# Kernel optimization log

Hardware: AMD Instinct MI355X
Metric: run time of the kernel (lower is better)

The kernel has to match this reference:

```python
import jax, jax.numpy as jnp
import numpy as np

N = 100000
E = 3200000
F_IN, H1, H2, C = 128, 64, 32, 10


def setup_inputs() -> dict:
    key = jax.random.key(0)
    ks = jax.random.split(key, 8)
    x = jax.random.normal(ks[0], (N, F_IN), dtype=jnp.float32)
    edge_index = jax.random.randint(ks[1], (2, E), 0, N, dtype=jnp.int64)
    W1 = jax.random.normal(ks[2], (F_IN, H1), dtype=jnp.float32) / np.sqrt(F_IN)
    b1 = jnp.zeros((H1,), dtype=jnp.float32)
    W2 = jax.random.normal(ks[3], (H1, H2), dtype=jnp.float32) / np.sqrt(H1)
    b2 = jnp.zeros((H2,), dtype=jnp.float32)
    Wc = jax.random.normal(ks[4], (H2, C), dtype=jnp.float32) / np.sqrt(H2)
    bc = jnp.zeros((C,), dtype=jnp.float32)
    return {"x": x, "edge_index": edge_index, "W1": W1, "b1": b1,
            "W2": W2, "b2": b2, "Wc": Wc, "bc": bc}


def gcn_conv(x, src, dst, W, b, n):
    # PyG GCNConv: x' = D^{-1/2} (A + I) D^{-1/2} (X W) + b
    h = x @ W                                        # [N, H]
    ones = jnp.ones((src.shape[0],), dtype=h.dtype)
    deg = jax.ops.segment_sum(ones, dst, num_segments=n) + 1.0  # +1 self loop
    dinv = jax.lax.rsqrt(deg)                        # deg >= 1, safe
    norm = dinv[src] * dinv[dst]                     # [E]
    msg = h[src] * norm[:, None]                     # [E, H] gather + scale
    agg = jax.ops.segment_sum(msg, dst, num_segments=n)
    # self-loop contribution: norm_ii = 1/deg_i
    out = agg + h * (dinv * dinv)[:, None]
    return out + b


def reference(x, edge_index, W1, b1, W2, b2, Wc, bc):
    n = x.shape[0]
    src, dst = edge_index[0], edge_index[1]
    h = gcn_conv(x, src, dst, W1, b1, n)
    h = jax.nn.relu(h)
    # dropout is identity in eval mode (training=False)
    h = gcn_conv(h, src, dst, W2, b2, n)
    h = jax.nn.relu(h)
    logits = h @ Wc + bc
    return jax.nn.log_softmax(logits, axis=1)
```

## Files before the change

### kernel.cpp

```cpp
#include <hip/hip_runtime.h>


#define BSHIFT 8
#define BMASK 255
#define NBUCK_MAX 512
#define TILE 4096
#define EPT 16

__device__ __forceinline__ unsigned pack_bf16(float lo, float hi) {
    unsigned ul = __float_as_uint(lo);
    ul = (ul + 0x7FFFu + ((ul >> 16) & 1u)) >> 16;
    unsigned uh = __float_as_uint(hi);
    uh = ((uh + 0x7FFFu + ((uh >> 16) & 1u)) >> 16) << 16;
    return ul | uh;
}

__global__ void k_hist(const int* __restrict__ dst, int* __restrict__ bcnt, int E) {
    __shared__ int h[NBUCK_MAX];
    for (int i = threadIdx.x; i < NBUCK_MAX; i += blockDim.x) h[i] = 0;
    __syncthreads();
    for (int e = blockIdx.x * blockDim.x + threadIdx.x; e < E; e += gridDim.x * blockDim.x)
        atomicAdd(&h[dst[e] >> BSHIFT], 1);
    __syncthreads();
    for (int i = threadIdx.x; i < NBUCK_MAX; i += blockDim.x)
        if (h[i]) atomicAdd(&bcnt[i], h[i]);
}

__global__ void k_scanb(const int* __restrict__ bcnt, int* __restrict__ bbase,
                        int* __restrict__ gcur, int E) {
    __shared__ int s[NBUCK_MAX];
    int t = threadIdx.x;
    int v = bcnt[t];
    s[t] = v;
    __syncthreads();
    for (int o = 1; o < NBUCK_MAX; o <<= 1) {
        int u = (t >= o) ? s[t - o] : 0;
        __syncthreads();
        s[t] += u;
        __syncthreads();
    }
    int ex = s[t] - v;
    bbase[t] = ex;
    gcur[t] = ex;
    if (t == NBUCK_MAX - 1) bbase[NBUCK_MAX] = E;
}

__global__ __launch_bounds__(256) void k_binA(const int* __restrict__ src,
                                              const int* __restrict__ dst,
                                              int* __restrict__ gcur,
                                              int* __restrict__ binned, int E) {
    __shared__ int hist[NBUCK_MAX];
    __shared__ int lbase[NBUCK_MAX];
    __shared__ int gdelta[NBUCK_MAX];
    __shared__ int cnt2[NBUCK_MAX];
    __shared__ int scanb[256];
    __shared__ int stage[TILE];
    __shared__ unsigned short sbucket[TILE];

    int t = threadIdx.x;
    for (int i = t; i < NBUCK_MAX; i += 256) { hist[i] = 0; cnt2[i] = 0; }
    __syncthreads();

    int tileStart = blockIdx.x * TILE;
    int cntTile = min(TILE, E - tileStart);

    int vals[EPT];
    int bks[EPT];
#pragma unroll
    for (int i = 0; i < EPT; i++) {
        int e = tileStart + t + i * 256;
        if (e < E) {
            int s = src[e], d = dst[e];
            vals[i] = s | ((d & BMASK) << 17);
            bks[i] = d >> BSHIFT;
            atomicAdd(&hist[bks[i]], 1);
        } else bks[i] = -1;
    }
    __syncthreads();

    int a0 = hist[2 * t], a1 = hist[2 * t + 1];
    int ts = a0 + a1;
    scanb[t] = ts;
    __syncthreads();
    for (int o = 1; o < 256; o <<= 1) {
        int u = (t >= o) ? scanb[t - o] : 0;
        __syncthreads();
        scanb[t] += u;
        __syncthreads();
    }
    int ex = scanb[t] - ts;
    lbase[2 * t] = ex;
    lbase[2 * t + 1] = ex + a0;
    __syncthreads();

    for (int b = t; b < NBUCK_MAX; b += 256) {
        int c = hist[b];
        int g = c ? atomicAdd(&gcur[b], c) : 0;
        gdelta[b] = g - lbase[b];
    }
#pragma unroll
    for (int i = 0; i < EPT; i++) {
        if (bks[i] >= 0) {
            int r = atomicAdd(&cnt2[bks[i]], 1);
            int slot = lbase[bks[i]] + r;
            stage[slot] = vals[i];
            sbucket[slot] = (unsigned short)bks[i];
        }
    }
    __syncthreads();
    for (int i = t; i < cntTile; i += 256) {
        int b = sbucket[i];
        binned[gdelta[b] + i] = stage[i];
    }
}

__global__ void k_rowptr(const int* __restrict__ bbase, const int* __restrict__ binned,
                         int* __restrict__ rowptr, float* __restrict__ dinv, int n, int E) {
    __shared__ int cnt[256];
    __shared__ int sc[256];
    int b = blockIdx.x, t = threadIdx.x;
    cnt[t] = 0;
    __syncthreads();
    int beg = bbase[b], end = bbase[b + 1];
    for (int i = beg + t; i < end; i += 256)
        atomicAdd(&cnt[(binned[i] >> 17) & BMASK], 1);
    __syncthreads();
    int v = cnt[t];
    sc[t] = v;
    __syncthreads();
    for (int o = 1; o < 256; o <<= 1) {
        int u = (t >= o) ? sc[t - o] : 0;
        __syncthreads();
        sc[t] += u;
        __syncthreads();
    }
    int g = (b << BSHIFT) + t;
    if (g < n) {
        rowptr[g] = beg + sc[t] - v;
        dinv[g] = rsqrtf((float)v + 1.0f);
        if (g == n - 1) rowptr[n] = E;
    }
}

__global__ void k_bucketsort(const int* __restrict__ bbase, const int* __restrict__ rowptr,
                             const int* __restrict__ binned, int* __restrict__ csr, int n) {
    __shared__ int rpl[256];
    __shared__ int lcur[256];
    int b = blockIdx.x, t = threadIdx.x;
    int lo = b << BSHIFT;
    int g = lo + t;
    rpl[t] = (g < n) ? rowptr[g] : 0;
    lcur[t] = 0;
    __syncthreads();
    int beg = bbase[b], end = bbase[b + 1];
    for (int i = beg + t; i < end; i += 256) {
        int v = binned[i];
        int ln = (v >> 17) & BMASK;
        int k = atomicAdd(&lcur[ln], 1);
        csr[rpl[ln] + k] = v & 0x1FFFF;
    }
}

template<int K, int M>
__global__ void k_gemm(const float* __restrict__ X, const float* __restrict__ W,
                       const float* __restrict__ dinv, unsigned* __restrict__ hsb, int n) {
    __shared__ float Ws[K * M];
    for (int i = threadIdx.x; i < K * M; i += blockDim.x) Ws[i] = W[i];
    __syncthreads();
    int r = blockIdx.x * blockDim.x + threadIdx.x;
    if (r >= n) return;
    float acc[M];
#pragma unroll
    for (int j = 0; j < M; j++) acc[j] = 0.f;
    const float* xr = X + (size_t)r * K;
    for (int k = 0; k < K; k += 4) {
        float4 xv = *(const float4*)(xr + k);
#pragma unroll
        for (int j = 0; j < M; j++) {
            acc[j] += xv.x * Ws[(k + 0) * M + j];
            acc[j] += xv.y * Ws[(k + 1) * M + j];
            acc[j] += xv.z * Ws[(k + 2) * M + j];
            acc[j] += xv.w * Ws[(k + 3) * M + j];
        }
    }
    float di = dinv[r];
    unsigned* hr = hsb + (size_t)r * (M / 2);
#pragma unroll
    for (int j = 0; j < M / 2; j++)
        hr[j] = pack_bf16(acc[2 * j] * di, acc[2 * j + 1] * di);
}

__global__ void k_agg64n(const int* __restrict__ rowptr, const int* __restrict__ csr,
                         const unsigned* __restrict__ hsb, const float* __restrict__ dinv,
                         const float* __restrict__ bv, float* __restrict__ out, int n) {
    int d = (blockIdx.x * blockDim.x + threadIdx.x) >> 6;
    if (d >= n) return;
    int lane = threadIdx.x & 63;
    int half = lane >> 5, l5 = lane & 31;
    int beg = rowptr[d], end = rowptr[d + 1];
    float di = dinv[d];
    float acc0 = 0.f, acc1 = 0.f;
    int base = beg;
    for (; base + 4 <= end; base += 4) {
        int sA = csr[base + half];
        int sB = csr[base + 2 + half];
        unsigned wA = hsb[(size_t)sA * 32 + l5];
        unsigned wB = hsb[(size_t)sB * 32 + l5];
        acc0 += __uint_as_float(wA << 16);
        acc1 += __uint_as_float(wA & 0xFFFF0000u);
        acc0 += __uint_as_float(wB << 16);
        acc1 += __uint_as_float(wB & 0xFFFF0000u);
    }
    for (int j = base + half; j < end; j += 2) {
        unsigned w = hsb[(size_t)csr[j] * 32 + l5];
        acc0 += __uint_as_float(w << 16);
        acc1 += __uint_as_float(w & 0xFFFF0000u);
    }
    acc0 += __shfl_xor(acc0, 32, 64);
    acc1 += __shfl_xor(acc1, 32, 64);
    if (half == 0) {
        unsigned ws = hsb[(size_t)d * 32 + l5];
        acc0 += __uint_as_float(ws << 16);
        acc1 += __uint_as_float(ws & 0xFFFF0000u);
        float v0 = fmaxf(acc0 * di + bv[2 * l5], 0.f);
        float v1 = fmaxf(acc1 * di + bv[2 * l5 + 1], 0.f);
        *(float2*)(out + (size_t)d * 64 + 2 * l5) = make_float2(v0, v1);
    }
}

__global__ void k_agg32n(const int* __restrict__ rowptr, const int* __restrict__ csr,
                         const unsigned* __restrict__ hsb, const float* __restrict__ dinv,
                         const float* __restrict__ bv, float* __restrict__ out, int n) {
    int d = (blockIdx.x * blockDim.x + threadIdx.x) >> 6;
    if (d >= n) return;
    int lane = threadIdx.x & 63;
    int quarter = lane >> 4, l4 = lane & 15;
    int beg = rowptr[d], end = rowptr[d + 1];
    float di = dinv[d];
    float acc0 = 0.f, acc1 = 0.f;
    int base = beg;
    for (; base + 8 <= end; base += 8) {
        int sA = csr[base + quarter];
        int sB = csr[base + 4 + quarter];
        unsigned wA = hsb[(size_t)sA * 16 + l4];
        unsigned wB = hsb[(size_t)sB * 16 + l4];
        acc0 += __uint_as_float(wA << 16);
        acc1 += __uint_as_float(wA & 0xFFFF0000u);
        acc0 += __uint_as_float(wB << 16);
        acc1 += __uint_as_float(wB & 0xFFFF0000u);
    }
    for (int j = base + quarter; j < end; j += 4) {
        unsigned w = hsb[(size_t)csr[j] * 16 + l4];
        acc0 += __uint_as_float(w << 16);
        acc1 += __uint_as_float(w & 0xFFFF0000u);
    }
    acc0 += __shfl_xor(acc0, 16, 64);
    acc1 += __shfl_xor(acc1, 16, 64);
    acc0 += __shfl_xor(acc0, 32, 64);
    acc1 += __shfl_xor(acc1, 32, 64);
    if (quarter == 0) {
        unsigned ws = hsb[(size_t)d * 16 + l4];
        acc0 += __uint_as_float(ws << 16);
        acc1 += __uint_as_float(ws & 0xFFFF0000u);
        float v0 = fmaxf(acc0 * di + bv[2 * l4], 0.f);
        float v1 = fmaxf(acc1 * di + bv[2 * l4 + 1], 0.f);
        *(float2*)(out + (size_t)d * 32 + 2 * l4) = make_float2(v0, v1);
    }
}

__global__ void k_classifier(const float* __restrict__ ACT, const float* __restrict__ Wc,
                             const float* __restrict__ bc, float* __restrict__ out, int n) {
    __shared__ float Wcs[32 * 10];
    __shared__ float bcs[10];
    for (int i = threadIdx.x; i < 320; i += blockDim.x) Wcs[i] = Wc[i];
    if (threadIdx.x < 10) bcs[threadIdx.x] = bc[threadIdx.x];
    __syncthreads();
    int r = blockIdx.x * blockDim.x + threadIdx.x;
    if (r >= n) return;
    const float* a = ACT + (size_t)r * 32;
    float logits[10];
#pragma unroll
    for (int c = 0; c < 10; c++) logits[c] = bcs[c];
#pragma unroll
    for (int k = 0; k < 32; k += 4) {
        float4 av = *(const float4*)(a + k);
#pragma unroll
        for (int c = 0; c < 10; c++) {
            logits[c] += av.x * Wcs[(k + 0) * 10 + c] + av.y * Wcs[(k + 1) * 10 + c]
                       + av.z * Wcs[(k + 2) * 10 + c] + av.w * Wcs[(k + 3) * 10 + c];
        }
    }
    float m = logits[0];
#pragma unroll
    for (int c = 1; c < 10; c++) m = fmaxf(m, logits[c]);
    float ssum = 0.f;
#pragma unroll
    for (int c = 0; c < 10; c++) ssum += __expf(logits[c] - m);
    float lse = m + __logf(ssum);
    float* o = out + (size_t)r * 10;
#pragma unroll
    for (int c = 0; c < 10; c++) o[c] = logits[c] - lse;
}

extern "C" void kernel_launch(void* const* d_in, const int* in_sizes, int n_in,
                              void* d_out, int out_size, void* d_ws, size_t ws_size,
                              hipStream_t stream) {
    const float* x  = (const float*)d_in[0];
    const int*   ei = (const int*)d_in[1];
    const float* W1 = (const float*)d_in[2];
    const float* b1 = (const float*)d_in[3];
    const float* W2 = (const float*)d_in[4];
    const float* b2 = (const float*)d_in[5];
    const float* Wc = (const float*)d_in[6];
    const float* bc = (const float*)d_in[7];
    float* out = (float*)d_out;

    const int N = in_sizes[0] / 128;
    const int E = in_sizes[1] / 2;
    const int* src = ei;
    const int* dst = ei + E;

    const int NBUCK = (N + BMASK) >> BSHIFT;
    const int NTILE = (E + TILE - 1) / TILE;

    char* ws = (char*)d_ws;
    size_t off = 0;
    auto alloc = [&](size_t elems) {
        void* p = ws + off;
        off += ((elems * 4 + 1023) & ~(size_t)1023);
        return p;
    };
    float*    dinv   = (float*)alloc(N);
    int*      bcnt   = (int*)alloc(NBUCK_MAX);
    int*      bbase  = (int*)alloc(NBUCK_MAX + 1);
    int*      gcur   = (int*)alloc(NBUCK_MAX);
    int*      rowptr = (int*)alloc(N + 1);
    int*      binned = (int*)alloc(E);
    int*      csr    = (int*)alloc(E);
    unsigned* hsb    = (unsigned*)alloc((size_t)N * 32);
    float*    act    = (float*)alloc((size_t)N * 64);

    hipMemsetAsync(bcnt, 0, sizeof(int) * NBUCK_MAX, stream);

    k_hist<<<512, 256, 0, stream>>>(dst, bcnt, E);
    k_scanb<<<1, NBUCK_MAX, 0, stream>>>(bcnt, bbase, gcur, E);
    k_binA<<<NTILE, 256, 0, stream>>>(src, dst, gcur, binned, E);
    k_rowptr<<<NBUCK, 256, 0, stream>>>(bbase, binned, rowptr, dinv, N, E);
    k_bucketsort<<<NBUCK, 256, 0, stream>>>(bbase, rowptr, binned, csr, N);

    k_gemm<128, 64><<<(N + 255) / 256, 256, 0, stream>>>(x, W1, dinv, hsb, N);
    k_agg64n<<<(N * 64 + 255) / 256, 256, 0, stream>>>(rowptr, csr, hsb, dinv, b1, act, N);

    k_gemm<64, 32><<<(N + 255) / 256, 256, 0, stream>>>(act, W2, dinv, hsb, N);
    k_agg32n<<<(N * 64 + 255) / 256, 256, 0, stream>>>(rowptr, csr, hsb, dinv, b2, act, N);

    k_classifier<<<(N + 255) / 256, 256, 0, stream>>>(act, Wc, bc, out, N);
}
```

Before: 429.6 us.

## Fuse rowptr and bucket sort, register-tile GEMM, vectorize aggregation gathers

```diff
diff --git a/kernel.cpp b/kernel.cpp
--- a/kernel.cpp
+++ b/kernel.cpp
@@ -101,8 +101,8 @@
 #pragma unroll
     for (int i = 0; i < EPT; i++) {
         if (bks[i] >= 0) {
-            int r = atomicAdd(&cnt2[bks[i]], 1);
-            int slot = lbase[bks[i]] + r;
+            int rr = atomicAdd(&cnt2[bks[i]], 1);
+            int slot = lbase[bks[i]] + rr;
             stage[slot] = vals[i];
             sbucket[slot] = (unsigned short)bks[i];
         }
@@ -114,12 +114,15 @@
     }
 }
 
-__global__ void k_rowptr(const int* __restrict__ bbase, const int* __restrict__ binned,
-                         int* __restrict__ rowptr, float* __restrict__ dinv, int n, int E) {
+__global__ void k_sortcsr(const int* __restrict__ bbase, const int* __restrict__ binned,
+                          int* __restrict__ rowptr, float* __restrict__ dinv,
+                          int* __restrict__ csr, int n, int E) {
     __shared__ int cnt[256];
     __shared__ int sc[256];
+    __shared__ int rpl[256];
+    __shared__ int lcur[256];
     int b = blockIdx.x, t = threadIdx.x;
-    cnt[t] = 0;
+    cnt[t] = 0; lcur[t] = 0;
     __syncthreads();
     int beg = bbase[b], end = bbase[b + 1];
     for (int i = beg + t; i < end; i += 256)
@@ -134,137 +137,213 @@
         sc[t] += u;
         __syncthreads();
     }
+    int rp = beg + sc[t] - v;
+    rpl[t] = rp;
     int g = (b << BSHIFT) + t;
     if (g < n) {
-        rowptr[g] = beg + sc[t] - v;
+        rowptr[g] = rp;
         dinv[g] = rsqrtf((float)v + 1.0f);
         if (g == n - 1) rowptr[n] = E;
     }
-}
-
-__global__ void k_bucketsort(const int* __restrict__ bbase, const int* __restrict__ rowptr,
-                             const int* __restrict__ binned, int* __restrict__ csr, int n) {
-    __shared__ int rpl[256];
-    __shared__ int lcur[256];
-    int b = blockIdx.x, t = threadIdx.x;
-    int lo = b << BSHIFT;
-    int g = lo + t;
-    rpl[t] = (g < n) ? rowptr[g] : 0;
-    lcur[t] = 0;
-    __syncthreads();
-    int beg = bbase[b], end = bbase[b + 1];
+    __syncthreads();
     for (int i = beg + t; i < end; i += 256) {
-        int v = binned[i];
-        int ln = (v >> 17) & BMASK;
+        int vv = binned[i];
+        int ln = (vv >> 17) & BMASK;
         int k = atomicAdd(&lcur[ln], 1);
-        csr[rpl[ln] + k] = v & 0x1FFFF;
+        csr[rpl[ln] + k] = vv & 0x1FFFF;
     }
 }
 
 template<int K, int M>
-__global__ void k_gemm(const float* __restrict__ X, const float* __restrict__ W,
-                       const float* __restrict__ dinv, unsigned* __restrict__ hsb, int n) {
+__global__ __launch_bounds__(256) void k_gemm(const float* __restrict__ X,
+                                              const float* __restrict__ W,
+                                              const float* __restrict__ dinv,
+                                              unsigned* __restrict__ hsb, int n) {
+    constexpr int MW = M / 4;
     __shared__ float Ws[K * M];
-    for (int i = threadIdx.x; i < K * M; i += blockDim.x) Ws[i] = W[i];
-    __syncthreads();
-    int r = blockIdx.x * blockDim.x + threadIdx.x;
-    if (r >= n) return;
-    float acc[M];
-#pragma unroll
-    for (int j = 0; j < M; j++) acc[j] = 0.f;
-    const float* xr = X + (size_t)r * K;
+    for (int i = threadIdx.x; i < K * M; i += 256) Ws[i] = W[i];
+    __syncthreads();
+    int w = threadIdx.x >> 6, lane = threadIdx.x & 63;
+    int wo = w * MW;
+    int r0 = blockIdx.x * 256 + lane;
+    float acc[4][MW];
+#pragma unroll
+    for (int i = 0; i < 4; i++)
+#pragma unroll
+        for (int j = 0; j < MW; j++) acc[i][j] = 0.f;
+
     for (int k = 0; k < K; k += 4) {
-        float4 xv = *(const float4*)(xr + k);
-#pragma unroll
-        for (int j = 0; j < M; j++) {
-            acc[j] += xv.x * Ws[(k + 0) * M + j];
-            acc[j] += xv.y * Ws[(k + 1) * M + j];
-            acc[j] += xv.z * Ws[(k + 2) * M + j];
-            acc[j] += xv.w * Ws[(k + 3) * M + j];
+        float4 xv[4];
+#pragma unroll
+        for (int i = 0; i < 4; i++) {
+            int rr = r0 + 64 * i;
+            xv[i] = (rr < n) ? *(const float4*)(X + (size_t)rr * K + k)
+                             : make_float4(0.f, 0.f, 0.f, 0.f);
         }
-    }
-    float di = dinv[r];
-    unsigned* hr = hsb + (size_t)r * (M / 2);
-#pragma unroll
-    for (int j = 0; j < M / 2; j++)
-        hr[j] = pack_bf16(acc[2 * j] * di, acc[2 * j + 1] * di);
+#pragma unroll
+        for (int kk = 0; kk < 4; kk++) {
+#pragma unroll
+            for (int j = 0; j < MW; j += 4) {
+                float4 wv = *(const float4*)&Ws[(k + kk) * M + wo + j];
+#pragma unroll
+                for (int i = 0; i < 4; i++) {
+                    float xs = (kk == 0) ? xv[i].x : (kk == 1) ? xv[i].y
+                             : (kk == 2) ? xv[i].z : xv[i].w;
+                    acc[i][j + 0] += xs * wv.x;
+                    acc[i][j + 1] += xs * wv.y;
+                    acc[i][j + 2] += xs * wv.z;
+                    acc[i][j + 3] += xs * wv.w;
+                }
+            }
+        }
+    }
+#pragma unroll
+    for (int i = 0; i < 4; i++) {
+        int rr = r0 + 64 * i;
+        if (rr < n) {
+            float di = dinv[rr];
+            unsigned p[MW / 2];
+#pragma unroll
+            for (int jj = 0; jj < MW / 2; jj++)
+                p[jj] = pack_bf16(acc[i][2 * jj] * di, acc[i][2 * jj + 1] * di);
+            unsigned* hr = hsb + (size_t)rr * (M / 2) + wo / 2;
+#pragma unroll
+            for (int jj = 0; jj < MW / 2; jj += 4)
+                *(uint4*)(hr + jj) = make_uint4(p[jj], p[jj + 1], p[jj + 2], p[jj + 3]);
+        }
+    }
 }
 
 __global__ void k_agg64n(const int* __restrict__ rowptr, const int* __restrict__ csr,
-                         const unsigned* __restrict__ hsb, const float* __restrict__ dinv,
+                         const uint4* __restrict__ hsb, const float* __restrict__ dinv,
                          const float* __restrict__ bv, float* __restrict__ out, int n) {
+    __shared__ float bs[64];
+    if (threadIdx.x < 64) bs[threadIdx.x] = bv[threadIdx.x];
+    __syncthreads();
     int d = (blockIdx.x * blockDim.x + threadIdx.x) >> 6;
     if (d >= n) return;
     int lane = threadIdx.x & 63;
-    int half = lane >> 5, l5 = lane & 31;
+    int q = lane >> 3;
+    int r = lane & 7;
     int beg = rowptr[d], end = rowptr[d + 1];
-    float di = dinv[d];
-    float acc0 = 0.f, acc1 = 0.f;
+    float acc[8];
+#pragma unroll
+    for (int i = 0; i < 8; i++) acc[i] = 0.f;
     int base = beg;
-    for (; base + 4 <= end; base += 4) {
-        int sA = csr[base + half];
-        int sB = csr[base + 2 + half];
-        unsigned wA = hsb[(size_t)sA * 32 + l5];
-        unsigned wB = hsb[(size_t)sB * 32 + l5];
-        acc0 += __uint_as_float(wA << 16);
-        acc1 += __uint_as_float(wA & 0xFFFF0000u);
-        acc0 += __uint_as_float(wB << 16);
-        acc1 += __uint_as_float(wB & 0xFFFF0000u);
-    }
-    for (int j = base + half; j < end; j += 2) {
-        unsigned w = hsb[(size_t)csr[j] * 32 + l5];
-        acc0 += __uint_as_float(w << 16);
-        acc1 += __uint_as_float(w & 0xFFFF0000u);
-    }
-    acc0 += __shfl_xor(acc0, 32, 64);
-    acc1 += __shfl_xor(acc1, 32, 64);
-    if (half == 0) {
-        unsigned ws = hsb[(size_t)d * 32 + l5];
-        acc0 += __uint_as_float(ws << 16);
-        acc1 += __uint_as_float(ws & 0xFFFF0000u);
-        float v0 = fmaxf(acc0 * di + bv[2 * l5], 0.f);
-        float v1 = fmaxf(acc1 * di + bv[2 * l5 + 1], 0.f);
-        *(float2*)(out + (size_t)d * 64 + 2 * l5) = make_float2(v0, v1);
+    for (; base + 16 <= end; base += 16) {
+        int sA = csr[base + q];
+        int sB = csr[base + 8 + q];
+        uint4 wA = hsb[(size_t)sA * 8 + r];
+        uint4 wB = hsb[(size_t)sB * 8 + r];
+        acc[0] += __uint_as_float(wA.x << 16);  acc[1] += __uint_as_float(wA.x & 0xFFFF0000u);
+        acc[2] += __uint_as_float(wA.y << 16);  acc[3] += __uint_as_float(wA.y & 0xFFFF0000u);
+        acc[4] += __uint_as_float(wA.z << 16);  acc[5] += __uint_as_float(wA.z & 0xFFFF0000u);
+        acc[6] += __uint_as_float(wA.w << 16);  acc[7] += __uint_as_float(wA.w & 0xFFFF0000u);
+        acc[0] += __uint_as_float(wB.x << 16);  acc[1] += __uint_as_float(wB.x & 0xFFFF0000u);
+        acc[2] += __uint_as_float(wB.y << 16);  acc[3] += __uint_as_float(wB.y & 0xFFFF0000u);
+        acc[4] += __uint_as_float(wB.z << 16);  acc[5] += __uint_as_float(wB.z & 0xFFFF0000u);
+        acc[6] += __uint_as_float(wB.w << 16);  acc[7] += __uint_as_float(wB.w & 0xFFFF0000u);
+    }
+    if (base + q < end) {
+        uint4 w = hsb[(size_t)csr[base + q] * 8 + r];
+        acc[0] += __uint_as_float(w.x << 16);  acc[1] += __uint_as_float(w.x & 0xFFFF0000u);
+        acc[2] += __uint_as_float(w.y << 16);  acc[3] += __uint_as_float(w.y & 0xFFFF0000u);
+        acc[4] += __uint_as_float(w.z << 16);  acc[5] += __uint_as_float(w.z & 0xFFFF0000u);
+        acc[6] += __uint_as_float(w.w << 16);  acc[7] += __uint_as_float(w.w & 0xFFFF0000u);
+    }
+    if (base + 8 + q < end) {
+        uint4 w = hsb[(size_t)csr[base + 8 + q] * 8 + r];
+        acc[0] += __uint_as_float(w.x << 16);  acc[1] += __uint_as_float(w.x & 0xFFFF0000u);
+        acc[2] += __uint_as_float(w.y << 16);  acc[3] += __uint_as_float(w.y & 0xFFFF0000u);
+        acc[4] += __uint_as_float(w.z << 16);  acc[5] += __uint_as_float(w.z & 0xFFFF0000u);
+        acc[6] += __uint_as_float(w.w << 16);  acc[7] += __uint_as_float(w.w & 0xFFFF0000u);
+    }
+#pragma unroll
+    for (int i = 0; i < 8; i++) {
+        acc[i] += __shfl_xor(acc[i], 8, 64);
+        acc[i] += __shfl_xor(acc[i], 16, 64);
+        acc[i] += __shfl_xor(acc[i], 32, 64);
+    }
+    uint4 ws = hsb[(size_t)d * 8 + r];
+    acc[0] += __uint_as_float(ws.x << 16);  acc[1] += __uint_as_float(ws.x & 0xFFFF0000u);
+    acc[2] += __uint_as_float(ws.y << 16);  acc[3] += __uint_as_float(ws.y & 0xFFFF0000u);
+    acc[4] += __uint_as_float(ws.z << 16);  acc[5] += __uint_as_float(ws.z & 0xFFFF0000u);
+    acc[6] += __uint_as_float(ws.w << 16);  acc[7] += __uint_as_float(ws.w & 0xFFFF0000u);
+    if (q == 0) {
+        float di = dinv[d];
+        float v[8];
+#pragma unroll
+        for (int i = 0; i < 8; i++) v[i] = fmaxf(acc[i] * di + bs[8 * r + i], 0.f);
+        float* o = out + (size_t)d * 64 + 8 * r;
+        *(float4*)(o + 0) = make_float4(v[0], v[1], v[2], v[3]);
+        *(float4*)(o + 4) = make_float4(v[4], v[5], v[6], v[7]);
     }
 }
 
 __global__ void k_agg32n(const int* __restrict__ rowptr, const int* __restrict__ csr,
-                         const unsigned* __restrict__ hsb, const float* __restrict__ dinv,
+                         const uint4* __restrict__ hsb, const float* __restrict__ dinv,
                          const float* __restrict__ bv, float* __restrict__ out, int n) {
+    __shared__ float bs[32];
+    if (threadIdx.x < 32) bs[threadIdx.x] = bv[threadIdx.x];
+    __syncthreads();
     int d = (blockIdx.x * blockDim.x + threadIdx.x) >> 6;
     if (d >= n) return;
     int lane = threadIdx.x & 63;
-    int quarter = lane >> 4, l4 = lane & 15;
+    int q = lane >> 2;
+    int r = lane & 3;
     int beg = rowptr[d], end = rowptr[d + 1];
-    float di = dinv[d];
-    float acc0 = 0.f, acc1 = 0.f;
+    float acc[8];
+#pragma unroll
+    for (int i = 0; i < 8; i++) acc[i] = 0.f;
     int base = beg;
-    for (; base + 8 <= end; base += 8) {
-        int sA = csr[base + quarter];
-        int sB = csr[base + 4 + quarter];
-        unsigned wA = hsb[(size_t)sA * 16 + l4];
-        unsigned wB = hsb[(size_t)sB * 16 + l4];
-        acc0 += __uint_as_float(wA << 16);
-        acc1 += __uint_as_float(wA & 0xFFFF0000u);
-        acc0 += __uint_as_float(wB << 16);
-        acc1 += __uint_as_float(wB & 0xFFFF0000u);
-    }
-    for (int j = base + quarter; j < end; j += 4) {
-        unsigned w = hsb[(size_t)csr[j] * 16 + l4];
-        acc0 += __uint_as_float(w << 16);
-        acc1 += __uint_as_float(w & 0xFFFF0000u);
-    }
-    acc0 += __shfl_xor(acc0, 16, 64);
-    acc1 += __shfl_xor(acc1, 16, 64);
-    acc0 += __shfl_xor(acc0, 32, 64);
-    acc1 += __shfl_xor(acc1, 32, 64);
-    if (quarter == 0) {
-        unsigned ws = hsb[(size_t)d * 16 + l4];
-        acc0 += __uint_as_float(ws << 16);
-        acc1 += __uint_as_float(ws & 0xFFFF0000u);
-        float v0 = fmaxf(acc0 * di + bv[2 * l4], 0.f);
-        float v1 = fmaxf(acc1 * di + bv[2 * l4 + 1], 0.f);
-        *(float2*)(out + (size_t)d * 32 + 2 * l4) = make_float2(v0, v1);
+    for (; base + 32 <= end; base += 32) {
+        int sA = csr[base + q];
+        int sB = csr[base + 16 + q];
+        uint4 wA = hsb[(size_t)sA * 4 + r];
+        uint4 wB = hsb[(size_t)sB * 4 + r];
+        acc[0] += __uint_as_float(wA.x << 16);  acc[1] += __uint_as_float(wA.x & 0xFFFF0000u);
+        acc[2] += __uint_as_float(wA.y << 16);  acc[3] += __uint_as_float(wA.y & 0xFFFF0000u);
+        acc[4] += __uint_as_float(wA.z << 16);  acc[5] += __uint_as_float(wA.z & 0xFFFF0000u);
+        acc[6] += __uint_as_float(wA.w << 16);  acc[7] += __uint_as_float(wA.w & 0xFFFF0000u);
+        acc[0] += __uint_as_float(wB.x << 16);  acc[1] += __uint_as_float(wB.x & 0xFFFF0000u);
+        acc[2] += __uint_as_float(wB.y << 16);  acc[3] += __uint_as_float(wB.y & 0xFFFF0000u);
+        acc[4] += __uint_as_float(wB.z << 16);  acc[5] += __uint_as_float(wB.z & 0xFFFF0000u);
+        acc[6] += __uint_as_float(wB.w << 16);  acc[7] += __uint_as_float(wB.w & 0xFFFF0000u);
+    }
+    if (base + q < end) {
+        uint4 w = hsb[(size_t)csr[base + q] * 4 + r];
+        acc[0] += __uint_as_float(w.x << 16);  acc[1] += __uint_as_float(w.x & 0xFFFF0000u);
+        acc[2] += __uint_as_float(w.y << 16);  acc[3] += __uint_as_float(w.y & 0xFFFF0000u);
+        acc[4] += __uint_as_float(w.z << 16);  acc[5] += __uint_as_float(w.z & 0xFFFF0000u);
+        acc[6] += __uint_as_float(w.w << 16);  acc[7] += __uint_as_float(w.w & 0xFFFF0000u);
+    }
+    if (base + 16 + q < end) {
+        uint4 w = hsb[(size_t)csr[base + 16 + q] * 4 + r];
+        acc[0] += __uint_as_float(w.x << 16);  acc[1] += __uint_as_float(w.x & 0xFFFF0000u);
+        acc[2] += __uint_as_float(w.y << 16);  acc[3] += __uint_as_float(w.y & 0xFFFF0000u);
+        acc[4] += __uint_as_float(w.z << 16);  acc[5] += __uint_as_float(w.z & 0xFFFF0000u);
+        acc[6] += __uint_as_float(w.w << 16);  acc[7] += __uint_as_float(w.w & 0xFFFF0000u);
+    }
+#pragma unroll
+    for (int i = 0; i < 8; i++) {
+        acc[i] += __shfl_xor(acc[i], 4, 64);
+        acc[i] += __shfl_xor(acc[i], 8, 64);
+        acc[i] += __shfl_xor(acc[i], 16, 64);
+        acc[i] += __shfl_xor(acc[i], 32, 64);
+    }
+    uint4 ws = hsb[(size_t)d * 4 + r];
+    acc[0] += __uint_as_float(ws.x << 16);  acc[1] += __uint_as_float(ws.x & 0xFFFF0000u);
+    acc[2] += __uint_as_float(ws.y << 16);  acc[3] += __uint_as_float(ws.y & 0xFFFF0000u);
+    acc[4] += __uint_as_float(ws.z << 16);  acc[5] += __uint_as_float(ws.z & 0xFFFF0000u);
+    acc[6] += __uint_as_float(ws.w << 16);  acc[7] += __uint_as_float(ws.w & 0xFFFF0000u);
+    if (q == 0) {
+        float di = dinv[d];
+        float v[8];
+#pragma unroll
+        for (int i = 0; i < 8; i++) v[i] = fmaxf(acc[i] * di + bs[8 * r + i], 0.f);
+        float* o = out + (size_t)d * 32 + 8 * r;
+        *(float4*)(o + 0) = make_float4(v[0], v[1], v[2], v[3]);
+        *(float4*)(o + 4) = make_float4(v[4], v[5], v[6], v[7]);
     }
 }
 
@@ -345,14 +424,15 @@
     k_hist<<<512, 256, 0, stream>>>(dst, bcnt, E);
     k_scanb<<<1, NBUCK_MAX, 0, stream>>>(bcnt, bbase, gcur, E);
     k_binA<<<NTILE, 256, 0, stream>>>(src, dst, gcur, binned, E);
-    k_rowptr<<<NBUCK, 256, 0, stream>>>(bbase, binned, rowptr, dinv, N, E);
-    k_bucketsort<<<NBUCK, 256, 0, stream>>>(bbase, rowptr, binned, csr, N);
+    k_sortcsr<<<NBUCK, 256, 0, stream>>>(bbase, binned, rowptr, dinv, csr, N, E);
 
     k_gemm<128, 64><<<(N + 255) / 256, 256, 0, stream>>>(x, W1, dinv, hsb, N);
-    k_agg64n<<<(N * 64 + 255) / 256, 256, 0, stream>>>(rowptr, csr, hsb, dinv, b1, act, N);
+    k_agg64n<<<(N * 64 + 255) / 256, 256, 0, stream>>>(rowptr, csr, (const uint4*)hsb,
+                                                       dinv, b1, act, N);
 
     k_gemm<64, 32><<<(N + 255) / 256, 256, 0, stream>>>(act, W2, dinv, hsb, N);
-    k_agg32n<<<(N * 64 + 255) / 256, 256, 0, stream>>>(rowptr, csr, hsb, dinv, b2, act, N);
+    k_agg32n<<<(N * 64 + 255) / 256, 256, 0, stream>>>(rowptr, csr, (const uint4*)hsb,
+                                                       dinv, b2, act, N);
 
     k_classifier<<<(N + 255) / 256, 256, 0, stream>>>(act, Wc, bc, out, N);
 }
```

Result: faster. 376.7 us (-12.3%).
